# Optimization experiments

Hardware: AMD Instinct MI355X
Metric: run time of the kernel (lower is better)

The kernel has to match this reference:

```python
import jax, jax.numpy as jnp
import numpy as np

DIMS, KS, NPOS = 128, 3, 8
B, H, W, NK = 4, 240, 320, 4000


def setup_inputs() -> dict:
    key = jax.random.key(0)
    ks = jax.random.split(key, 8)
    x = jax.random.normal(ks[0], (B, DIMS, H, W), jnp.float32)
    # keypoints normalized to [-1,1] (module maps them to pixel coords)
    keypoints = jax.random.uniform(ks[1], (B, NK, 2), jnp.float32, minval=-0.95, maxval=0.95)
    w1 = jax.random.normal(ks[2], (2 * NPOS, DIMS, KS, KS), jnp.float32) * 0.05
    b1 = jax.random.normal(ks[3], (2 * NPOS,), jnp.float32) * 0.05
    w2 = jax.random.normal(ks[4], (2 * NPOS, 2 * NPOS), jnp.float32) * 0.2
    b2 = jax.random.normal(ks[5], (2 * NPOS,), jnp.float32) * 0.05
    sf_w = jax.random.normal(ks[6], (DIMS, DIMS), jnp.float32) * 0.05
    agg_w = jax.random.uniform(ks[7], (NPOS, DIMS, DIMS), jnp.float32)  # torch.rand init
    return dict(x=x, keypoints=keypoints, w1=w1, b1=b1, w2=w2, b2=b2, sf_w=sf_w, agg_w=agg_w)


def _get_patches(xi, cx, cy, ps):
    # xi: [c,h,w]; cx,cy: [N] int top-left corners -> patches [N,c,ps,ps]
    off = jnp.arange(ps)
    iy = cy[:, None, None] + off[None, :, None]  # [N,ps,1]
    ix = cx[:, None, None] + off[None, None, :]  # [N,1,ps]
    return xi[:, iy, ix].transpose(1, 0, 2, 3)


def _bilinear_zeros(xi, px, py):
    # grid_sample bilinear, padding_mode='zeros', align_corners=True; px,py pixel coords [M]
    c, h, w = xi.shape
    x0 = jnp.floor(px)
    y0 = jnp.floor(py)
    wx = px - x0
    wy = py - y0

    def gat(xc, yc):
        valid = (xc >= 0) & (xc <= w - 1) & (yc >= 0) & (yc <= h - 1)
        xi_c = jnp.clip(xc, 0, w - 1).astype(jnp.int32)
        yi_c = jnp.clip(yc, 0, h - 1).astype(jnp.int32)
        return xi[:, yi_c, xi_c] * valid.astype(xi.dtype)  # [c,M]

    return (gat(x0, y0) * (1 - wx) * (1 - wy)
            + gat(x0 + 1, y0) * wx * (1 - wy)
            + gat(x0, y0 + 1) * (1 - wx) * wy
            + gat(x0 + 1, y0 + 1) * wx * wy)


def _sddh_one(xi, kpts, w1, b1, w2, b2, sf_w, agg_w):
    c, h, w = xi.shape
    wh = jnp.array([w - 1, h - 1], jnp.float32)
    max_off = max(h, w) / 4.0
    kw = (kpts / 2.0 + 0.5) * wh                       # [N,2] pixel coords (x,y)
    kwl = kw.astype(jnp.int32)                          # .long() trunc (coords >=0 -> floor)
    corner = (kwl.astype(jnp.float32) - KS / 2 + 1).astype(jnp.int32)
    cx = jnp.clip(corner[:, 0], 0, w - 1 - KS)
    cy = jnp.clip(corner[:, 1], 0, h - 1 - KS)
    patch = _get_patches(xi, cx, cy, KS)                # [N,c,ks,ks]
    # offset_conv: 3x3 valid conv on 3x3 patch == full contraction, then ReLU, then 1x1 conv
    o = jnp.einsum('ncij,ocij->no', patch, w1) + b1
    o = jax.nn.relu(o)
    o = o @ w2.T + b2                                   # [N, 2*NPOS]
    o = jnp.clip(o, -max_off, max_off)
    offset = o.reshape(-1, 2, NPOS).transpose(0, 2, 1)  # [N,NPOS,2] (x,y)
    pos = kw[:, None, :] + offset                       # sample positions in pixels
    # (the module normalizes to [-1,1] then grid_sample(align_corners=True) unnormalizes back)
    feats = _bilinear_zeros(xi, pos[..., 0].reshape(-1), pos[..., 1].reshape(-1))
    feats = feats.reshape(c, -1, NPOS).transpose(1, 0, 2)  # [N,c,NPOS]
    feats = jax.nn.selu(jnp.einsum('dc,ncp->ndp', sf_w, feats))  # sf_conv 1x1 + selu
    descs = jnp.einsum('ncp,pcd->nd', feats, agg_w)
    norm = jnp.linalg.norm(descs, axis=1, keepdims=True)
    return descs / jnp.maximum(norm, 1e-12)             # F.normalize p=2 dim=1


def reference(x, keypoints, w1, b1, w2, b2, sf_w, agg_w):
    return jax.vmap(_sddh_one, in_axes=(0, 0, None, None, None, None, None, None))(
        x, keypoints, w1, b1, w2, b2, sf_w, agg_w)  # [B,NK,DIMS]
```

## Files before the change

kernel.cpp:

```cpp
#include <hip/hip_runtime.h>
#include <cstdint>
#include <cmath>

#define BB   4
#define NK   4000
#define NKP  (BB*NK)
#define CH   128
#define HH   240
#define WW   320
#define HWSZ (HH*WW)
#define NPOS 8

typedef __attribute__((ext_vector_type(8))) short short8;
typedef __attribute__((ext_vector_type(8))) unsigned short ushort8;
typedef __attribute__((ext_vector_type(4))) float f32x4;

static constexpr size_t OFF_POS  = 32768000;
static constexpr size_t OFF_SFT  = 65536000;
static constexpr size_t OFF_W1T  = 65601536;
static constexpr size_t OFF_XCL  = 65675264;
static constexpr size_t OFF_SFB  = 222961664;
static constexpr size_t OFF_AGB  = 222994432;
static constexpr size_t WS_FULL  = 223256576;
static constexpr size_t WS_MIN   = 65675264;

__device__ __forceinline__ unsigned short f2bf(float f) {
    unsigned int u = __float_as_uint(f);
    u += 0x7fff + ((u >> 16) & 1);
    return (unsigned short)(u >> 16);
}
__device__ __forceinline__ float bf2f(unsigned short u) {
    return __uint_as_float((unsigned)u << 16);
}

__global__ __launch_bounds__(256) void k_prep(const float* __restrict__ sfw,
                                              const float* __restrict__ w1,
                                              const float* __restrict__ aggw,
                                              float* __restrict__ sfT,
                                              float* __restrict__ w1T,
                                              unsigned short* __restrict__ sfB,
                                              unsigned short* __restrict__ agB)
{
    int id = blockIdx.x * 256 + threadIdx.x;
    if (id < 16384) {
        int cc = id >> 7, dd = id & 127;
        sfT[cc * 128 + dd] = sfw[dd * 128 + cc];
    } else if (id < 16384 + 18432) {
        int j = id - 16384;
        int o = j / 1152, r = j % 1152;
        int k = r >> 7, c = r & 127;
        w1T[j] = w1[o * 1152 + c * 9 + k];
    } else if (id < 16384 + 18432 + 16384) {
        int idx = id - (16384 + 18432);
        int j = idx & 7, lane = (idx >> 3) & 63, nt = (idx >> 9) & 7, kc32 = (idx >> 12) & 3;
        int k = kc32 * 32 + (lane >> 4) * 8 + j;
        int n = nt * 16 + (lane & 15);
        sfB[idx] = f2bf(sfw[n * 128 + k]);
    } else if (id < 16384 + 18432 + 16384 + 131072) {
        int idx = id - (16384 + 18432 + 16384);
        int local = idx & 16383, kc = idx >> 14;
        int j = local & 7, lane = (local >> 3) & 63, nt = (local >> 9) & 7, kc32 = (local >> 12) & 3;
        int k = kc * 128 + kc32 * 32 + (lane >> 4) * 8 + j;
        int n = nt * 16 + (lane & 15);
        agB[idx] = f2bf(aggw[(size_t)k * 128 + n]);
    }
}

__global__ __launch_bounds__(256) void k_tr(const float* __restrict__ x,
                                            unsigned short* __restrict__ xclb)
{
    const int b  = blockIdx.y;
    const int p0 = blockIdx.x * 64;
    const int t  = threadIdx.x;
    __shared__ float tile[64 * 129];

    #pragma unroll
    for (int i = 0; i < 8; ++i) {
        int flat = i * 256 + t;
        int c  = flat >> 4;
        int p4 = flat & 15;
        float4 v = *(const float4*)(x + ((size_t)(b * 128 + c)) * HWSZ + p0 + p4 * 4);
        tile[(p4 * 4 + 0) * 129 + c] = v.x;
        tile[(p4 * 4 + 1) * 129 + c] = v.y;
        tile[(p4 * 4 + 2) * 129 + c] = v.z;
        tile[(p4 * 4 + 3) * 129 + c] = v.w;
    }
    __syncthreads();
    #pragma unroll
    for (int j = 0; j < 4; ++j) {
        int flat = j * 256 + t;
        int p  = flat >> 4;
        int c8 = flat & 15;
        ushort8 o;
        #pragma unroll
        for (int k = 0; k < 8; ++k)
            o[k] = f2bf(tile[p * 129 + c8 * 8 + k]);
        *(ushort8*)(xclb + ((size_t)b * HWSZ + p0 + p) * CH + c8 * 8) = o;
    }
}

__global__ __launch_bounds__(256, 4) void k_mega(
    const unsigned short* __restrict__ xclb, const float* __restrict__ kp,
    const float* __restrict__ w1T, const float* __restrict__ b1,
    const float* __restrict__ w2,  const float* __restrict__ b2,
    const unsigned short* __restrict__ sfB,
    const unsigned short* __restrict__ agB,
    float* __restrict__ out)
{
    const int t  = threadIdx.x;
    const int n0 = blockIdx.x * 16;
    const int bi = n0 / NK;

    __shared__ __align__(16) char U[37376];
    float* wl = (float*)U;
    unsigned short* plb = (unsigned short*)(U + 24832);
    char*  GlB = U;
    float* Dl = (float*)U;
    __shared__ float  o1l[16 * 16];
    __shared__ float  kwl[16 * 2];
    __shared__ int2   cxyl[16];
    __shared__ float2 posl[128];

    if (t < 16) {
        const int n = n0 + t;
        float kx = kp[2 * n], ky = kp[2 * n + 1];
        float kwx = (kx * 0.5f + 0.5f) * (float)(WW - 1);
        float kwy = (ky * 0.5f + 0.5f) * (float)(HH - 1);
        kwl[t * 2 + 0] = kwx;
        kwl[t * 2 + 1] = kwy;
        int cx = (int)((float)((int)kwx) - 0.5f);
        int cy = (int)((float)((int)kwy) - 0.5f);
        cx = min(max(cx, 0), WW - 4);
        cy = min(max(cy, 0), HH - 4);
        cxyl[t] = make_int2(cx, cy);
    }
    __syncthreads();

    const int o_c  = t >> 4;
    const int kp_c = t & 15;
    float acc0 = 0.f, acc1 = 0.f;
    const unsigned short* xb = xclb + (size_t)bi * HWSZ * CH;

    for (int h = 0; h < 3; ++h) {
        if (h) __syncthreads();
        #pragma unroll
        for (int i = 0; i < 6; ++i) {
            int idx = i * 256 + t;
            int o = idx / 96, c4 = idx % 96;
            *(float4*)&wl[o * 388 + c4 * 4] =
                *(const float4*)&w1T[o * 1152 + h * 384 + c4 * 4];
        }
        #pragma unroll
        for (int i = 0; i < 3; ++i) {
            int idx = i * 256 + t;
            int kk = idx / 48, r = idx % 48;
            int px = r >> 4, c8 = r & 15;
            int2 c = cxyl[kk];
            ushort8 raw = *(const ushort8*)(xb + ((size_t)(c.y + h) * WW + (c.x + px)) * CH + c8 * 8);
            *(ushort8*)&plb[kk * 392 + px * 128 + c8 * 8] = raw;
        }
        __syncthreads();
        #pragma unroll 4
        for (int g = 0; g < 48; ++g) {
            float4 w0  = *(const float4*)&wl[o_c * 388 + g * 8];
            float4 w1v = *(const float4*)&wl[o_c * 388 + g * 8 + 4];
            ushort8 p8 = *(const ushort8*)&plb[kp_c * 392 + g * 8];
            acc0 = fmaf(w0.x, bf2f(p8[0]), fmaf(w0.y, bf2f(p8[1]),
                   fmaf(w0.z, bf2f(p8[2]), fmaf(w0.w, bf2f(p8[3]), acc0))));
            acc1 = fmaf(w1v.x, bf2f(p8[4]), fmaf(w1v.y, bf2f(p8[5]),
                   fmaf(w1v.z, bf2f(p8[6]), fmaf(w1v.w, bf2f(p8[7]), acc1))));
        }
    }

    __syncthreads();
    o1l[kp_c * 16 + o_c] = fmaxf(acc0 + acc1 + b1[o_c], 0.f);
    __syncthreads();

    if (t < 128) {
        const int kk = t >> 3, j = t & 7;
        float sx = b2[j], sy = b2[8 + j];
        #pragma unroll
        for (int i = 0; i < 16; ++i) {
            float v = o1l[kk * 16 + i];
            sx = fmaf(v, w2[j * 16 + i], sx);
            sy = fmaf(v, w2[(8 + j) * 16 + i], sy);
        }
        sx = fminf(fmaxf(sx, -80.f), 80.f);
        sy = fminf(fmaxf(sy, -80.f), 80.f);
        posl[kk * 8 + j] = make_float2(kwl[kk * 2 + 0] + sx, kwl[kk * 2 + 1] + sy);
    }
    __syncthreads();

    const int w = t >> 6, l = t & 63;
    const int fr = l & 15, fq = l >> 4;

    for (int chunk = 0; chunk < 2; ++chunk) {
        const int arow = chunk * 64 + w * 16 + fr;
        float2 P = posl[arow];
        const float x0 = floorf(P.x), y0 = floorf(P.y);
        const float wx = P.x - x0, wy = P.y - y0;
        const unsigned short* cp[4];
        float cw[4];
        #pragma unroll
        for (int dy = 0; dy < 2; ++dy) {
            const float yc = y0 + (float)dy;
            const bool vy = (yc >= 0.f) && (yc <= (float)(HH - 1));
            const int  yi = (int)fminf(fmaxf(yc, 0.f), (float)(HH - 1));
            const float wyv = dy ? wy : (1.f - wy);
            #pragma unroll
            for (int dx = 0; dx < 2; ++dx) {
                const float xc = x0 + (float)dx;
                const bool vx = (xc >= 0.f) && (xc <= (float)(WW - 1));
                const int  xi = (int)fminf(fmaxf(xc, 0.f), (float)(WW - 1));
                cp[dy * 2 + dx] = xb + ((size_t)yi * WW + xi) * CH;
                cw[dy * 2 + dx] = (vx && vy) ? (dx ? wx : (1.f - wx)) * wyv : 0.f;
            }
        }

        short8 a[4];
        #pragma unroll
        for (int q = 0; q < 4; ++q) {
            const int ch = q * 32 + fq * 8;
            ushort8 c0 = *(const ushort8*)(cp[0] + ch);
            ushort8 c1 = *(const ushort8*)(cp[1] + ch);
            ushort8 c2 = *(const ushort8*)(cp[2] + ch);
            ushort8 c3 = *(const ushort8*)(cp[3] + ch);
            short8 av;
            #pragma unroll
            for (int j = 0; j < 8; ++j) {
                float s = fmaf(bf2f(c0[j]), cw[0], 0.f);
                s = fmaf(bf2f(c1[j]), cw[1], s);
                s = fmaf(bf2f(c2[j]), cw[2], s);
                s = fmaf(bf2f(c3[j]), cw[3], s);
                av[j] = (short)f2bf(s);
            }
            a[q] = av;
        }

        f32x4 acc[8];
        #pragma unroll
        for (int nt = 0; nt < 8; ++nt)
            #pragma unroll
            for (int r = 0; r < 4; ++r) acc[nt][r] = 0.f;

        #pragma unroll 2
        for (int nt = 0; nt < 8; ++nt) {
            short8 b[4];
            #pragma unroll
            for (int q = 0; q < 4; ++q)
                b[q] = *(const short8*)(sfB + ((size_t)(q * 8 + nt) * 64 + l) * 8);
            #pragma unroll
            for (int q = 0; q < 4; ++q)
                acc[nt] = __builtin_amdgcn_mfma_f32_16x16x32_bf16(a[q], b[q], acc[nt], 0, 0, 0);
        }

        #pragma unroll
        for (int nt = 0; nt < 8; ++nt)
            #pragma unroll
            for (int r = 0; r < 4; ++r) {
                float v = acc[nt][r];
                float e = v > 0.f ? v : 1.6732632423543772f * (__expf(v) - 1.f);
                const int row = chunk * 64 + w * 16 + fq * 4 + r;
                unsigned byte = (unsigned)(row * 256 + (nt * 16 + fr) * 2);
                byte ^= ((unsigned)((row >> 3) & 7)) << 4;
                *(unsigned short*)(GlB + byte) = f2bf(1.0507009873554805f * e);
            }
    }
    __syncthreads();

    f32x4 acc2[2];
    #pragma unroll
    for (int i = 0; i < 2; ++i)
        #pragma unroll
        for (int r = 0; r < 4; ++r) acc2[i][r] = 0.f;

    const int nt0 = w * 2;
    #pragma unroll 4
    for (int kk = 0; kk < 32; ++kk) {
        const int row = fr * 8 + (kk >> 2);
        unsigned byte = (unsigned)(row * 256 + ((kk & 3) * 32 + fq * 8) * 2);
        byte ^= ((unsigned)((row >> 3) & 7)) << 4;
        short8 a2 = *(const short8*)(GlB + byte);
        #pragma unroll
        for (int i = 0; i < 2; ++i) {
            short8 b2 = *(const short8*)(agB + (size_t)(kk >> 2) * 16384 +
                ((size_t)(((kk & 3) * 8 + nt0 + i) * 64 + l)) * 8);
            acc2[i] = __builtin_amdgcn_mfma_f32_16x16x32_bf16(a2, b2, acc2[i], 0, 0, 0);
        }
    }

    __syncthreads();
    #pragma unroll
    for (int i = 0; i < 2; ++i)
        #pragma unroll
        for (int r = 0; r < 4; ++r)
            Dl[(fq * 4 + r) * 132 + w * 32 + i * 16 + fr] = acc2[i][r];
    __syncthreads();

    {
        const int row = t >> 4, seg = t & 15;
        const float* dr = Dl + row * 132 + seg * 8;
        float4 d0 = *(const float4*)(dr);
        float4 d1 = *(const float4*)(dr + 4);
        float s = d0.x*d0.x + d0.y*d0.y + d0.z*d0.z + d0.w*d0.w
                + d1.x*d1.x + d1.y*d1.y + d1.z*d1.z + d1.w*d1.w;
        #pragma unroll
        for (int m = 1; m < 16; m <<= 1) s += __shfl_xor(s, m);
        const float inv = 1.f / fmaxf(sqrtf(s), 1e-12f);
        float* op = out + (size_t)(n0 + row) * 128 + seg * 8;
        float4 o0 = {d0.x*inv, d0.y*inv, d0.z*inv, d0.w*inv};
        float4 o1 = {d1.x*inv, d1.y*inv, d1.z*inv, d1.w*inv};
        *(float4*)(op)     = o0;
        *(float4*)(op + 4) = o1;
    }
}

__global__ __launch_bounds__(128) void k_sample(
    const float* __restrict__ x,  const float* __restrict__ kp,
    const float* __restrict__ w1, const float* __restrict__ b1,
    const float* __restrict__ w2, const float* __restrict__ b2,
    float* __restrict__ feats)
{
    const int n  = blockIdx.x;
    const int bi = n / NK;
    const int t  = threadIdx.x;

    __shared__ __align__(16) float patch[CH * 9];
    __shared__ float red[16 * 8];
    __shared__ float o1[16];
    __shared__ float offv[16];

    const float kx  = kp[(size_t)n * 2 + 0];
    const float ky  = kp[(size_t)n * 2 + 1];
    const float kwx = (kx * 0.5f + 0.5f) * (float)(WW - 1);
    const float kwy = (ky * 0.5f + 0.5f) * (float)(HH - 1);
    const int kwlx = (int)kwx;
    const int kwly = (int)kwy;
    int cx = (int)((float)kwlx - 0.5f);
    int cy = (int)((float)kwly - 0.5f);
    cx = min(max(cx, 0), WW - 1 - 3);
    cy = min(max(cy, 0), HH - 1 - 3);

    const float* xb = x + ((size_t)bi * CH + t) * HWSZ;
    {
        const float* p0 = xb + cy * WW + cx;
        #pragma unroll
        for (int i = 0; i < 3; ++i) {
            patch[t * 9 + i * 3 + 0] = p0[i * WW + 0];
            patch[t * 9 + i * 3 + 1] = p0[i * WW + 1];
            patch[t * 9 + i * 3 + 2] = p0[i * WW + 2];
        }
    }
    __syncthreads();
    {
        const int o = t & 15, g = t >> 4;
        const float4* wp = (const float4*)(w1 + o * 1152 + g * 144);
        const float4* pp = (const float4*)(patch + g * 144);
        float s = 0.f;
        #pragma unroll
        for (int q = 0; q < 36; ++q) {
            float4 wv = wp[q];
            float4 pv = pp[q];
            s = fmaf(wv.x, pv.x, fmaf(wv.y, pv.y, fmaf(wv.z, pv.z, fmaf(wv.w, pv.w, s))));
        }
        red[o * 8 + g] = s;
    }
    __syncthreads();
    if (t < 16) {
        float s = b1[t];
        #pragma unroll
        for (int g = 0; g < 8; ++g) s += red[t * 8 + g];
        o1[t] = fmaxf(s, 0.f);
    }
    __syncthreads();
    if (t < 16) {
        float s = b2[t];
        #pragma unroll
        for (int j = 0; j < 16; ++j) s = fmaf(o1[j], w2[t * 16 + j], s);
        offv[t] = fminf(fmaxf(s, -80.f), 80.f);
    }
    __syncthreads();

    #pragma unroll
    for (int p = 0; p < NPOS; ++p) {
        const float px = kwx + offv[p];
        const float py = kwy + offv[8 + p];
        const float x0 = floorf(px), y0 = floorf(py);
        const float wx = px - x0, wy = py - y0;
        float acc = 0.f;
        #pragma unroll
        for (int dy = 0; dy < 2; ++dy) {
            const float yc = y0 + (float)dy;
            const bool vy = (yc >= 0.f) && (yc <= (float)(HH - 1));
            const int  yi = (int)fminf(fmaxf(yc, 0.f), (float)(HH - 1));
            const float wyv = dy ? wy : (1.f - wy);
            #pragma unroll
            for (int dx = 0; dx < 2; ++dx) {
                const float xc = x0 + (float)dx;
                const bool vx = (xc >= 0.f) && (xc <= (float)(WW - 1));
                const int  xi = (int)fminf(fmaxf(xc, 0.f), (float)(WW - 1));
                const float wxv = dx ? wx : (1.f - wx);
                float v = xb[yi * WW + xi];
                v = (vx && vy) ? v : 0.f;
                acc = fmaf(v, wxv * wyv, acc);
            }
        }
        feats[((size_t)n * 8 + p) * CH + t] = acc;
    }
}

__global__ __launch_bounds__(256) void k_sf_legacy(float* __restrict__ gbuf,
                                                   const float* __restrict__ sfT)
{
    const int m0 = blockIdx.x * 64;
    const int t  = threadIdx.x;
    __shared__ __align__(16) float AT[128 * 68];

    #pragma unroll
    for (int i = 0; i < 32; ++i) {
        int flat = i * 256 + t;
        int mm = flat >> 7, kk = flat & 127;
        AT[kk * 68 + mm] = gbuf[(size_t)(m0 + mm) * 128 + kk];
    }
    __syncthreads();

    const int tx = t & 31, ty = t >> 5;
    const int d0 = tx * 4, mb = ty * 8;
    float acc[8][4];
    #pragma unroll
    for (int i = 0; i < 8; ++i)
        #pragma unroll
        for (int j = 0; j < 4; ++j) acc[i][j] = 0.f;

    #pragma unroll 4
    for (int k = 0; k < 128; ++k) {
        float4 a0 = *(const float4*)(AT + k * 68 + mb);
        float4 a1 = *(const float4*)(AT + k * 68 + mb + 4);
        float4 bq = *(const float4*)(sfT + k * 128 + d0);
        float a[8] = {a0.x, a0.y, a0.z, a0.w, a1.x, a1.y, a1.z, a1.w};
        float b4[4] = {bq.x, bq.y, bq.z, bq.w};
        #pragma unroll
        for (int i = 0; i < 8; ++i)
            #pragma unroll
            for (int j = 0; j < 4; ++j)
                acc[i][j] = fmaf(a[i], b4[j], acc[i][j]);
    }

    #pragma unroll
    for (int i = 0; i < 8; ++i) {
        float4 o;
        float* ov = &o.x;
        #pragma unroll
        for (int j = 0; j < 4; ++j) {
            float v = acc[i][j];
            float r = v > 0.f ? v : 1.6732632423543772f * expm1f(v);
            ov[j] = 1.0507009873554805f * r;
        }
        *(float4*)(gbuf + (size_t)(m0 + mb + i) * 128 + d0) = o;
    }
}

__global__ __launch_bounds__(256) void k_agg_mono(const float* __restrict__ gbuf,
                                                  const float* __restrict__ aggw,
                                                  float* __restrict__ out)
{
    const int m0 = blockIdx.x * 64;
    const int t  = threadIdx.x;
    __shared__ __align__(16) float AT[128 * 68];

    const int tx = t & 31, ty = t >> 5;
    const int d0 = tx * 4, mb = ty * 8;
    float acc[8][4];
    #pragma unroll
    for (int i = 0; i < 8; ++i)
        #pragma unroll
        for (int j = 0; j < 4; ++j) acc[i][j] = 0.f;

    for (int kc = 0; kc < 8; ++kc) {
        __syncthreads();
        #pragma unroll
        for (int i = 0; i < 32; ++i) {
            int flat = i * 256 + t;
            int mm = flat >> 7, kk = flat & 127;
            AT[kk * 68 + mm] = gbuf[(size_t)(m0 + mm) * 1024 + kc * 128 + kk];
        }
        __syncthreads();
        #pragma unroll 4
        for (int kk = 0; kk < 128; ++kk) {
            float4 a0 = *(const float4*)(AT + kk * 68 + mb);
            float4 a1 = *(const float4*)(AT + kk * 68 + mb + 4);
            float4 bq = *(const float4*)(aggw + (size_t)(kc * 128 + kk) * 128 + d0);
            float a[8] = {a0.x, a0.y, a0.z, a0.w, a1.x, a1.y, a1.z, a1.w};
            float b4[4] = {bq.x, bq.y, bq.z, bq.w};
            #pragma unroll
            for (int i = 0; i < 8; ++i)
                #pragma unroll
                for (int j = 0; j < 4; ++j)
                    acc[i][j] = fmaf(a[i], b4[j], acc[i][j]);
        }
    }

    #pragma unroll
    for (int i = 0; i < 8; ++i) {
        float s = acc[i][0] * acc[i][0] + acc[i][1] * acc[i][1]
                + acc[i][2] * acc[i][2] + acc[i][3] * acc[i][3];
        #pragma unroll
        for (int m = 16; m; m >>= 1) s += __shfl_xor(s, m);
        const float inv = 1.f / fmaxf(sqrtf(s), 1e-12f);
        float4 o = {acc[i][0] * inv, acc[i][1] * inv, acc[i][2] * inv, acc[i][3] * inv};
        *(float4*)(out + (size_t)(m0 + mb + i) * 128 + d0) = o;
    }
}

extern "C" void kernel_launch(void* const* d_in, const int* in_sizes, int n_in,
                              void* d_out, int out_size, void* d_ws, size_t ws_size,
                              hipStream_t stream)
{
    const float* x   = (const float*)d_in[0];
    const float* kp  = (const float*)d_in[1];
    const float* w1  = (const float*)d_in[2];
    const float* b1  = (const float*)d_in[3];
    const float* w2  = (const float*)d_in[4];
    const float* b2  = (const float*)d_in[5];
    const float* sfw = (const float*)d_in[6];
    const float* agg = (const float*)d_in[7];
    float* out = (float*)d_out;

    if (ws_size < WS_MIN) return;

    char*  ws    = (char*)d_ws;
    float* sfT   = (float*)(ws + OFF_SFT);
    float* w1T   = (float*)(ws + OFF_W1T);
    unsigned short* xclb = (unsigned short*)(ws + OFF_XCL);
    unsigned short* sfB  = (unsigned short*)(ws + OFF_SFB);
    unsigned short* agB  = (unsigned short*)(ws + OFF_AGB);

    k_prep<<<712, 256, 0, stream>>>(sfw, w1, agg, sfT, w1T, sfB, agB);

    if (ws_size >= WS_FULL) {
        dim3 grid(HWSZ / 64, BB);
        k_tr  <<<grid, 256, 0, stream>>>(x, xclb);
        k_mega<<<NKP / 16, 256, 0, stream>>>(xclb, kp, w1T, b1, w2, b2, sfB, agB, out);
    } else {
        float* feats = (float*)ws;
        k_sample   <<<NKP, 128, 0, stream>>>(x, kp, w1, b1, w2, b2, feats);
        k_sf_legacy<<<2000, 256, 0, stream>>>(feats, sfT);
        k_agg_mono <<<250,  256, 0, stream>>>(feats, agg, out);
    }
}
```

Before: 301.3 us.

## Compute offset conv with bf16 MFMA and fold weight prep into transpose kernel

The 3x3 offset convolution moves from scalar FMAs over three staged row passes to a single staged 16x1152 patch and 36 bf16 MFMA 16x16x32 instructions, with w1 pre-packed into an MFMA B-fragment layout in bf16. The weight-prep kernel is merged into the transpose kernel as extra blocks, which removes one launch. An extra barrier guards the shared buffer reuse. The conv weights now lose precision by going to bf16, and all four waves compute the same MFMA even though only one writes the result.

```diff
diff --git a/kernel.cpp b/kernel.cpp
--- a/kernel.cpp
+++ b/kernel.cpp
@@ -33,75 +33,72 @@
     return __uint_as_float((unsigned)u << 16);
 }
 
-__global__ __launch_bounds__(256) void k_prep(const float* __restrict__ sfw,
-                                              const float* __restrict__ w1,
-                                              const float* __restrict__ aggw,
-                                              float* __restrict__ sfT,
-                                              float* __restrict__ w1T,
-                                              unsigned short* __restrict__ sfB,
-                                              unsigned short* __restrict__ agB)
-{
-    int id = blockIdx.x * 256 + threadIdx.x;
-    if (id < 16384) {
-        int cc = id >> 7, dd = id & 127;
-        sfT[cc * 128 + dd] = sfw[dd * 128 + cc];
-    } else if (id < 16384 + 18432) {
-        int j = id - 16384;
-        int o = j / 1152, r = j % 1152;
-        int k = r >> 7, c = r & 127;
-        w1T[j] = w1[o * 1152 + c * 9 + k];
-    } else if (id < 16384 + 18432 + 16384) {
-        int idx = id - (16384 + 18432);
-        int j = idx & 7, lane = (idx >> 3) & 63, nt = (idx >> 9) & 7, kc32 = (idx >> 12) & 3;
-        int k = kc32 * 32 + (lane >> 4) * 8 + j;
-        int n = nt * 16 + (lane & 15);
-        sfB[idx] = f2bf(sfw[n * 128 + k]);
-    } else if (id < 16384 + 18432 + 16384 + 131072) {
-        int idx = id - (16384 + 18432 + 16384);
-        int local = idx & 16383, kc = idx >> 14;
-        int j = local & 7, lane = (local >> 3) & 63, nt = (local >> 9) & 7, kc32 = (local >> 12) & 3;
-        int k = kc * 128 + kc32 * 32 + (lane >> 4) * 8 + j;
-        int n = nt * 16 + (lane & 15);
-        agB[idx] = f2bf(aggw[(size_t)k * 128 + n]);
-    }
-}
-
-__global__ __launch_bounds__(256) void k_tr(const float* __restrict__ x,
-                                            unsigned short* __restrict__ xclb)
-{
-    const int b  = blockIdx.y;
-    const int p0 = blockIdx.x * 64;
-    const int t  = threadIdx.x;
+__global__ __launch_bounds__(256) void k_trprep(
+    const float* __restrict__ x,   unsigned short* __restrict__ xclb,
+    const float* __restrict__ sfw, const float* __restrict__ w1,
+    const float* __restrict__ aggw,
+    unsigned short* __restrict__ sfB, unsigned short* __restrict__ agB,
+    unsigned short* __restrict__ w1B)
+{
+    const int t = threadIdx.x;
     __shared__ float tile[64 * 129];
 
-    #pragma unroll
-    for (int i = 0; i < 8; ++i) {
-        int flat = i * 256 + t;
-        int c  = flat >> 4;
-        int p4 = flat & 15;
-        float4 v = *(const float4*)(x + ((size_t)(b * 128 + c)) * HWSZ + p0 + p4 * 4);
-        tile[(p4 * 4 + 0) * 129 + c] = v.x;
-        tile[(p4 * 4 + 1) * 129 + c] = v.y;
-        tile[(p4 * 4 + 2) * 129 + c] = v.z;
-        tile[(p4 * 4 + 3) * 129 + c] = v.w;
-    }
-    __syncthreads();
-    #pragma unroll
-    for (int j = 0; j < 4; ++j) {
-        int flat = j * 256 + t;
-        int p  = flat >> 4;
-        int c8 = flat & 15;
-        ushort8 o;
-        #pragma unroll
-        for (int k = 0; k < 8; ++k)
-            o[k] = f2bf(tile[p * 129 + c8 * 8 + k]);
-        *(ushort8*)(xclb + ((size_t)b * HWSZ + p0 + p) * CH + c8 * 8) = o;
+    if (blockIdx.x < 4800) {
+        const int b  = blockIdx.x / 1200;
+        const int p0 = (blockIdx.x % 1200) * 64;
+        #pragma unroll
+        for (int i = 0; i < 8; ++i) {
+            int flat = i * 256 + t;
+            int c  = flat >> 4;
+            int p4 = flat & 15;
+            float4 v = *(const float4*)(x + ((size_t)(b * 128 + c)) * HWSZ + p0 + p4 * 4);
+            tile[(p4 * 4 + 0) * 129 + c] = v.x;
+            tile[(p4 * 4 + 1) * 129 + c] = v.y;
+            tile[(p4 * 4 + 2) * 129 + c] = v.z;
+            tile[(p4 * 4 + 3) * 129 + c] = v.w;
+        }
+        __syncthreads();
+        #pragma unroll
+        for (int j = 0; j < 4; ++j) {
+            int flat = j * 256 + t;
+            int p  = flat >> 4;
+            int c8 = flat & 15;
+            ushort8 o;
+            #pragma unroll
+            for (int k = 0; k < 8; ++k)
+                o[k] = f2bf(tile[p * 129 + c8 * 8 + k]);
+            *(ushort8*)(xclb + ((size_t)b * HWSZ + p0 + p) * CH + c8 * 8) = o;
+        }
+    } else {
+        int id = (blockIdx.x - 4800) * 256 + t;
+        if (id < 16384) {
+            int idx = id;
+            int j = idx & 7, lane = (idx >> 3) & 63, nt = (idx >> 9) & 7, kc32 = (idx >> 12) & 3;
+            int k = kc32 * 32 + (lane >> 4) * 8 + j;
+            int n = nt * 16 + (lane & 15);
+            sfB[idx] = f2bf(sfw[n * 128 + k]);
+        } else if (id < 16384 + 131072) {
+            int idx = id - 16384;
+            int local = idx & 16383, kc = idx >> 14;
+            int j = local & 7, lane = (local >> 3) & 63, nt = (local >> 9) & 7, kc32 = (local >> 12) & 3;
+            int k = kc * 128 + kc32 * 32 + (lane >> 4) * 8 + j;
+            int n = nt * 16 + (lane & 15);
+            agB[idx] = f2bf(aggw[(size_t)k * 128 + n]);
+        } else if (id < 16384 + 131072 + 18432) {
+            int e = id - (16384 + 131072);
+            int j = e & 7, l = (e >> 3) & 63, q = e >> 9;
+            int k = q * 32 + ((l >> 4) & 3) * 8 + j;
+            int o = l & 15;
+            int h = k / 384, rem = k % 384;
+            int px = rem >> 7, c = rem & 127;
+            w1B[e] = f2bf(w1[o * 1152 + c * 9 + (h * 3 + px)]);
+        }
     }
 }
 
 __global__ __launch_bounds__(256, 4) void k_mega(
     const unsigned short* __restrict__ xclb, const float* __restrict__ kp,
-    const float* __restrict__ w1T, const float* __restrict__ b1,
+    const unsigned short* __restrict__ w1B, const float* __restrict__ b1,
     const float* __restrict__ w2,  const float* __restrict__ b2,
     const unsigned short* __restrict__ sfB,
     const unsigned short* __restrict__ agB,
@@ -110,10 +107,11 @@
     const int t  = threadIdx.x;
     const int n0 = blockIdx.x * 16;
     const int bi = n0 / NK;
-
-    __shared__ __align__(16) char U[37376];
-    float* wl = (float*)U;
-    unsigned short* plb = (unsigned short*)(U + 24832);
+    const int w  = t >> 6, l = t & 63;
+    const int fr = l & 15, fq = l >> 4;
+
+    __shared__ __align__(16) char U[37120];
+    unsigned short* plb = (unsigned short*)U;
     char*  GlB = U;
     float* Dl = (float*)U;
     __shared__ float  o1l[16 * 16];
@@ -136,44 +134,37 @@
     }
     __syncthreads();
 
-    const int o_c  = t >> 4;
-    const int kp_c = t & 15;
-    float acc0 = 0.f, acc1 = 0.f;
     const unsigned short* xb = xclb + (size_t)bi * HWSZ * CH;
 
-    for (int h = 0; h < 3; ++h) {
-        if (h) __syncthreads();
-        #pragma unroll
-        for (int i = 0; i < 6; ++i) {
-            int idx = i * 256 + t;
-            int o = idx / 96, c4 = idx % 96;
-            *(float4*)&wl[o * 388 + c4 * 4] =
-                *(const float4*)&w1T[o * 1152 + h * 384 + c4 * 4];
-        }
-        #pragma unroll
-        for (int i = 0; i < 3; ++i) {
-            int idx = i * 256 + t;
-            int kk = idx / 48, r = idx % 48;
-            int px = r >> 4, c8 = r & 15;
-            int2 c = cxyl[kk];
-            ushort8 raw = *(const ushort8*)(xb + ((size_t)(c.y + h) * WW + (c.x + px)) * CH + c8 * 8);
-            *(ushort8*)&plb[kk * 392 + px * 128 + c8 * 8] = raw;
-        }
-        __syncthreads();
+    #pragma unroll
+    for (int i = 0; i < 9; ++i) {
+        int idx = i * 256 + t;
+        int kk = idx / 144, rr = idx % 144;
+        int oe = rr * 8;
+        int h = oe / 384, rem = oe % 384;
+        int px = rem >> 7, c0 = rem & 127;
+        int2 c = cxyl[kk];
+        *(ushort8*)&plb[kk * 1160 + oe] =
+            *(const ushort8*)(xb + ((size_t)(c.y + h) * WW + (c.x + px)) * CH + c0);
+    }
+    __syncthreads();
+
+    {
+        f32x4 ca;
+        #pragma unroll
+        for (int r = 0; r < 4; ++r) ca[r] = 0.f;
         #pragma unroll 4
-        for (int g = 0; g < 48; ++g) {
-            float4 w0  = *(const float4*)&wl[o_c * 388 + g * 8];
-            float4 w1v = *(const float4*)&wl[o_c * 388 + g * 8 + 4];
-            ushort8 p8 = *(const ushort8*)&plb[kp_c * 392 + g * 8];
-            acc0 = fmaf(w0.x, bf2f(p8[0]), fmaf(w0.y, bf2f(p8[1]),
-                   fmaf(w0.z, bf2f(p8[2]), fmaf(w0.w, bf2f(p8[3]), acc0))));
-            acc1 = fmaf(w1v.x, bf2f(p8[4]), fmaf(w1v.y, bf2f(p8[5]),
-                   fmaf(w1v.z, bf2f(p8[6]), fmaf(w1v.w, bf2f(p8[7]), acc1))));
-        }
-    }
-
-    __syncthreads();
-    o1l[kp_c * 16 + o_c] = fmaxf(acc0 + acc1 + b1[o_c], 0.f);
+        for (int q = 0; q < 36; ++q) {
+            short8 a = *(const short8*)(plb + fr * 1160 + q * 32 + fq * 8);
+            short8 b = *(const short8*)(w1B + (size_t)(q * 64 + l) * 8);
+            ca = __builtin_amdgcn_mfma_f32_16x16x32_bf16(a, b, ca, 0, 0, 0);
+        }
+        if (w == 0) {
+            #pragma unroll
+            for (int r = 0; r < 4; ++r)
+                o1l[(fq * 4 + r) * 16 + fr] = fmaxf(ca[r] + b1[fr], 0.f);
+        }
+    }
     __syncthreads();
 
     if (t < 128) {
@@ -190,9 +181,6 @@
         posl[kk * 8 + j] = make_float2(kwl[kk * 2 + 0] + sx, kwl[kk * 2 + 1] + sy);
     }
     __syncthreads();
-
-    const int w = t >> 6, l = t & 63;
-    const int fr = l & 15, fq = l >> 4;
 
     for (int chunk = 0; chunk < 2; ++chunk) {
         const int arow = chunk * 64 + w * 16 + fr;
@@ -254,6 +242,7 @@
                 acc[nt] = __builtin_amdgcn_mfma_f32_16x16x32_bf16(a[q], b[q], acc[nt], 0, 0, 0);
         }
 
+        if (chunk == 0) __syncthreads();
         #pragma unroll
         for (int nt = 0; nt < 8; ++nt)
             #pragma unroll
@@ -312,6 +301,16 @@
         float4 o1 = {d1.x*inv, d1.y*inv, d1.z*inv, d1.w*inv};
         *(float4*)(op)     = o0;
         *(float4*)(op + 4) = o1;
+    }
+}
+
+__global__ __launch_bounds__(256) void k_prep_legacy(const float* __restrict__ sfw,
+                                                     float* __restrict__ sfT)
+{
+    int id = blockIdx.x * 256 + threadIdx.x;
+    if (id < 16384) {
+        int cc = id >> 7, dd = id & 127;
+        sfT[cc * 128 + dd] = sfw[dd * 128 + cc];
     }
 }
 
@@ -530,19 +529,17 @@
 
     char*  ws    = (char*)d_ws;
     float* sfT   = (float*)(ws + OFF_SFT);
-    float* w1T   = (float*)(ws + OFF_W1T);
+    unsigned short* w1B  = (unsigned short*)(ws + OFF_W1T);
     unsigned short* xclb = (unsigned short*)(ws + OFF_XCL);
     unsigned short* sfB  = (unsigned short*)(ws + OFF_SFB);
     unsigned short* agB  = (unsigned short*)(ws + OFF_AGB);
 
-    k_prep<<<712, 256, 0, stream>>>(sfw, w1, agg, sfT, w1T, sfB, agB);
-
     if (ws_size >= WS_FULL) {
-        dim3 grid(HWSZ / 64, BB);
-        k_tr  <<<grid, 256, 0, stream>>>(x, xclb);
-        k_mega<<<NKP / 16, 256, 0, stream>>>(xclb, kp, w1T, b1, w2, b2, sfB, agB, out);
+        k_trprep<<<5448, 256, 0, stream>>>(x, xclb, sfw, w1, agg, sfB, agB, w1B);
+        k_mega  <<<NKP / 16, 256, 0, stream>>>(xclb, kp, w1B, b1, w2, b2, sfB, agB, out);
     } else {
         float* feats = (float*)ws;
+        k_prep_legacy<<<64, 256, 0, stream>>>(sfw, sfT);
         k_sample   <<<NKP, 128, 0, stream>>>(x, kp, w1, b1, w2, b2, feats);
         k_sf_legacy<<<2000, 256, 0, stream>>>(feats, sfT);
         k_agg_mono <<<250,  256, 0, stream>>>(feats, agg, out);
```

Result: faster. 290.9 us (-3.5%).
